# Kernel tuning notes

Measured on AMD Instinct MI355X. Metric: run time of the kernel, lower is better.

Reference implementation:

```python
import jax, jax.numpy as jnp
import numpy as np

BERT_DIM, HIDDEN, LABELS, UFD = 768, 256, 9, 20
B, R, S = 64, 16, 64


def _masked_mean(x, mask, axis):
    # x: [..., axis, d], mask: [..., axis] float 0/1 -> masked mean over `axis`
    num = jnp.sum(x * mask[..., None], axis=axis)
    den = jnp.maximum(jnp.sum(mask, axis=axis), 1e-9)[..., None]
    return num / den


def setup_inputs() -> dict:
    key = jax.random.key(0)
    ks = jax.random.split(key, 8)
    sc = 0.02
    return {
        "inputs": jax.random.normal(ks[0], (B, R, S, BERT_DIM), jnp.float32),
        "user_feats": jax.random.normal(ks[1], (B, UFD), jnp.float32),
        "W_proj": jax.random.normal(ks[2], (BERT_DIM, HIDDEN), jnp.float32) * sc,
        "b_proj": jnp.zeros((HIDDEN,), jnp.float32),
        "W_rff": jax.random.normal(ks[3], (HIDDEN + UFD, 1), jnp.float32) * sc,
        "b_rff": jnp.zeros((1,), jnp.float32),
        "W_pff": jax.random.normal(ks[4], (HIDDEN + UFD, LABELS), jnp.float32) * sc,
        "b_pff": jnp.zeros((LABELS,), jnp.float32),
        "user_w": jnp.ones((UFD,), jnp.float32),
    }


def reference(inputs, user_feats, W_proj, b_proj, W_rff, b_rff, W_pff, b_pff, user_w):
    # projection: [B,R,S,bert] -> [B,R,S,H]
    x = jnp.einsum("brsd,dh->brsh", inputs, W_proj) + b_proj
    # sentence-level DAN: mask = sum over hidden != 0 (as in source, post-projection)
    s_mask = (jnp.sum(x, axis=-1) != 0).astype(x.dtype)          # [B,R,S]
    r_hn = _masked_mean(x, s_mask, axis=2)                        # [B,R,H]
    # review-level DAN
    r_mask = (jnp.sum(x, axis=(-1, -2)) != 0).astype(x.dtype)    # [B,R]
    p_hn = _masked_mean(r_hn, r_mask, axis=1)                     # [B,H]
    # F.normalize(user_feats) (L2 over dim=1, eps=1e-12) scaled by learned weights
    nrm = jnp.maximum(jnp.linalg.norm(user_feats, axis=1, keepdims=True), 1e-12)
    uf = (user_feats / nrm) * user_w
    p_batch = jnp.concatenate([p_hn, uf], axis=-1)                # [B,H+UFD]
    # review feedforward (Linear -> SELU), squeezed -> [B]
    r_stars = jax.nn.selu(p_batch @ W_rff + b_rff)[:, 0]
    # product DAN over the batch axis (no mask -> plain mean), then Linear+SELU
    h_n = jnp.mean(p_batch, axis=0)                               # [H+UFD]
    p_stars = jax.nn.selu(h_n @ W_pff + b_pff)                    # [LABELS]
    return p_stars, r_stars
```

## Files before the change

kernel.cpp:

```cpp
#include <hip/hip_runtime.h>
#include <cmath>

static constexpr int BERT   = 768;
static constexpr int HID    = 256;
static constexpr int NLAB   = 9;
static constexpr int NUFD   = 20;
static constexpr int NB     = 64;
static constexpr int NR     = 16;
static constexpr int NS     = 64;
static constexpr int PBD    = HID + NUFD;

static constexpr size_t WS_A      = 0;
static constexpr size_t WS_COLSUM = 786432;
static constexpr size_t WS_SUMB   = 787200;
static constexpr size_t WS_CNT    = 787264;
static constexpr size_t WS_TSUM   = 788288;
static constexpr size_t WS_PB     = 789312;

__device__ __forceinline__ float selu_f(float x) {
    const float alpha = 1.6732632423543772848170429916717f;
    const float scale = 1.0507009873554804934193349852946f;
    return scale * (x > 0.0f ? x : alpha * (expf(x) - 1.0f));
}

__global__ __launch_bounds__(256) void k0_colsum(
    const float* __restrict__ W, const float* __restrict__ bp,
    float* __restrict__ colsum, float* __restrict__ sumb) {
    int blk = blockIdx.x;
    int tid = threadIdx.x;
    if (blk < 3) {
        int d = blk * 256 + tid;
        const float4* W4 = (const float4*)W;
        float4 s4 = make_float4(0.f, 0.f, 0.f, 0.f);
        for (int h4 = 0; h4 < HID / 4; ++h4) {
            float4 v = W4[(size_t)d * (HID / 4) + h4];
            s4.x += v.x; s4.y += v.y; s4.z += v.z; s4.w += v.w;
        }
        colsum[d] = (s4.x + s4.y) + (s4.z + s4.w);
    } else {
        __shared__ float red[256];
        red[tid] = bp[tid];
        __syncthreads();
        for (int s = 128; s > 0; s >>= 1) {
            if (tid < s) red[tid] += red[tid + s];
            __syncthreads();
        }
        if (tid == 0) *sumb = red[0];
    }
}

__global__ __launch_bounds__(256) void k1_reduce(
    const float* __restrict__ inp, const float* __restrict__ colsum,
    const float* __restrict__ sumb, float* __restrict__ A,
    float* __restrict__ cnt_g, float* __restrict__ tsum_g) {
    int br  = blockIdx.x;
    int tid = threadIdx.x;
    int w = tid >> 6, l = tid & 63;

    const float4* cs4 = (const float4*)colsum;
    float4 c0 = cs4[l], c1 = cs4[64 + l], c2 = cs4[128 + l];
    float sb = *sumb;

    const float4* base = (const float4*)(inp + (size_t)br * NS * BERT);
    float4 a0 = make_float4(0.f,0.f,0.f,0.f);
    float4 a1 = make_float4(0.f,0.f,0.f,0.f);
    float4 a2 = make_float4(0.f,0.f,0.f,0.f);
    float cnt = 0.f, ts = 0.f;

    #pragma unroll 4
    for (int i = 0; i < 16; ++i) {
        int s = w * 16 + i;
        const float4* rp = base + (size_t)s * (BERT / 4);
        float4 v0 = rp[l];
        float4 v1 = rp[64 + l];
        float4 v2 = rp[128 + l];
        float p = v0.x*c0.x + v0.y*c0.y + v0.z*c0.z + v0.w*c0.w
                + v1.x*c1.x + v1.y*c1.y + v1.z*c1.z + v1.w*c1.w
                + v2.x*c2.x + v2.y*c2.y + v2.z*c2.z + v2.w*c2.w;
        #pragma unroll
        for (int off = 32; off > 0; off >>= 1) p += __shfl_xor(p, off);
        float t = p + sb;
        ts += t;
        if (t != 0.0f) {
            a0.x += v0.x; a0.y += v0.y; a0.z += v0.z; a0.w += v0.w;
            a1.x += v1.x; a1.y += v1.y; a1.z += v1.z; a1.w += v1.w;
            a2.x += v2.x; a2.y += v2.y; a2.z += v2.z; a2.w += v2.w;
            cnt += 1.0f;
        }
    }

    __shared__ float part[4][BERT];
    __shared__ float cw[4], tw[4];
    float* pw = part[w];
    ((float4*)pw)[l]       = a0;
    ((float4*)pw)[64 + l]  = a1;
    ((float4*)pw)[128 + l] = a2;
    if (l == 0) { cw[w] = cnt; tw[w] = ts; }
    __syncthreads();

    float* Ao = A + (size_t)br * BERT;
    for (int c = tid; c < BERT; c += 256)
        Ao[c] = (part[0][c] + part[1][c]) + (part[2][c] + part[3][c]);
    if (tid == 0) {
        cnt_g[br]  = (cw[0] + cw[1]) + (cw[2] + cw[3]);
        tsum_g[br] = (tw[0] + tw[1]) + (tw[2] + tw[3]);
    }
}

__global__ __launch_bounds__(256) void k2_perb(
    const float* __restrict__ A, const float* __restrict__ cnt_g,
    const float* __restrict__ tsum_g, const float* __restrict__ W_proj,
    const float* __restrict__ b_proj, const float* __restrict__ user_feats,
    const float* __restrict__ user_w, const float* __restrict__ W_rff,
    const float* __restrict__ b_rff, float* __restrict__ pb_out,
    float* __restrict__ r_out) {
    int b   = blockIdx.x;
    int tid = threadIdx.x;

    __shared__ float M[BERT];
    __shared__ float g[NR];
    __shared__ float scal[4];
    __shared__ float pb[PBD];
    __shared__ float red[256];

    if (tid < NR) {
        float c  = cnt_g[b * NR + tid];
        float t  = tsum_g[b * NR + tid];
        float rm = (t != 0.0f) ? 1.0f : 0.0f;
        float den = fmaxf(c, 1e-9f);
        g[tid]       = rm / den;
        red[tid]     = rm;
        red[16 + tid] = rm * (c / den);
    }
    __syncthreads();
    if (tid == 0) {
        float srm = 0.f, sq = 0.f;
        for (int r = 0; r < NR; ++r) { srm += red[r]; sq += red[16 + r]; }
        scal[0] = fmaxf(srm, 1e-9f);
        scal[1] = sq;
    }
    for (int c = tid; c < BERT; c += 256) {
        float m = 0.f;
        #pragma unroll
        for (int r = 0; r < NR; ++r)
            m += g[r] * A[(size_t)(b * NR + r) * BERT + c];
        M[c] = m;
    }
    __syncthreads();

    float acc = 0.f;
    {
        const float* Wc = W_proj + tid;
        #pragma unroll 8
        for (int d = 0; d < BERT; ++d) acc += M[d] * Wc[(size_t)d * HID];
    }
    pb[tid] = (acc + b_proj[tid] * scal[1]) / scal[0];

    if (tid < NUFD) red[tid] = user_feats[b * NUFD + tid];
    __syncthreads();
    if (tid == 0) {
        float s = 0.f;
        for (int j = 0; j < NUFD; ++j) s += red[j] * red[j];
        scal[2] = 1.0f / fmaxf(sqrtf(s), 1e-12f);
    }
    __syncthreads();
    if (tid < NUFD) pb[HID + tid] = red[tid] * scal[2] * user_w[tid];
    __syncthreads();

    pb_out[b * PBD + tid] = pb[tid];
    if (tid < PBD - HID) pb_out[b * PBD + HID + tid] = pb[HID + tid];

    float part = pb[tid] * W_rff[tid];
    if (tid < PBD - HID) part += pb[HID + tid] * W_rff[HID + tid];
    red[tid] = part;
    __syncthreads();
    for (int s = 128; s > 0; s >>= 1) {
        if (tid < s) red[tid] += red[tid + s];
        __syncthreads();
    }
    if (tid == 0) r_out[b] = selu_f(red[0] + b_rff[0]);
}

__global__ __launch_bounds__(320) void k3_final(
    const float* __restrict__ pb, const float* __restrict__ W_pff,
    const float* __restrict__ b_pff, float* __restrict__ out) {
    __shared__ float hn[PBD];
    int tid = threadIdx.x;
    if (tid < PBD) {
        float s = 0.f;
        for (int b = 0; b < NB; ++b) s += pb[b * PBD + tid];
        hn[tid] = s * (1.0f / NB);
    }
    __syncthreads();
    if (tid < NLAB) {
        float acc = 0.f;
        for (int j = 0; j < PBD; ++j) acc += hn[j] * W_pff[j * NLAB + tid];
        out[tid] = selu_f(acc + b_pff[tid]);
    }
}

extern "C" void kernel_launch(void* const* d_in, const int* in_sizes, int n_in,
                              void* d_out, int out_size, void* d_ws, size_t ws_size,
                              hipStream_t stream) {
    const float* inputs     = (const float*)d_in[0];
    const float* user_feats = (const float*)d_in[1];
    const float* W_proj     = (const float*)d_in[2];
    const float* b_proj     = (const float*)d_in[3];
    const float* W_rff      = (const float*)d_in[4];
    const float* b_rff      = (const float*)d_in[5];
    const float* W_pff      = (const float*)d_in[6];
    const float* b_pff      = (const float*)d_in[7];
    const float* user_w     = (const float*)d_in[8];
    float* out = (float*)d_out;
    float* ws  = (float*)d_ws;

    float* A      = ws + WS_A;
    float* colsum = ws + WS_COLSUM;
    float* sumb   = ws + WS_SUMB;
    float* cntg   = ws + WS_CNT;
    float* tsumg  = ws + WS_TSUM;
    float* pb     = ws + WS_PB;

    hipLaunchKernelGGL(k0_colsum, dim3(4), dim3(256), 0, stream,
                       W_proj, b_proj, colsum, sumb);
    hipLaunchKernelGGL(k1_reduce, dim3(NB * NR), dim3(256), 0, stream,
                       inputs, colsum, sumb, A, cntg, tsumg);
    hipLaunchKernelGGL(k2_perb, dim3(NB), dim3(256), 0, stream,
                       A, cntg, tsumg, W_proj, b_proj, user_feats, user_w,
                       W_rff, b_rff, pb, out + NLAB);
    hipLaunchKernelGGL(k3_final, dim3(1), dim3(320), 0, stream,
                       pb, W_pff, b_pff, out);
}
```

Measured before the change: 345.1 us.

## Split per-batch projection GEMV across four blocks and use nontemporal input loads

The per-batch projection kernel now runs four blocks per batch row. Each block computes 64 hidden outputs, with a 4-way split-K over the 768 input dims reduced in shared memory, replacing one block doing a full 768-long loop per thread. The review feedforward (r_stars) moves into the final single-block kernel, computed by 64 threads. The main streaming reduction reads inputs with nontemporal loads and uses native vector types. This raises parallelism in the small GEMV stage but recomputes the M vector four times per batch row.

```diff
diff --git a/kernel.cpp b/kernel.cpp
--- a/kernel.cpp
+++ b/kernel.cpp
@@ -10,6 +10,8 @@
 static constexpr int NS     = 64;
 static constexpr int PBD    = HID + NUFD;
 
+typedef float v4f __attribute__((ext_vector_type(4)));
+
 static constexpr size_t WS_A      = 0;
 static constexpr size_t WS_COLSUM = 786432;
 static constexpr size_t WS_SUMB   = 787200;
@@ -30,12 +32,11 @@
     int tid = threadIdx.x;
     if (blk < 3) {
         int d = blk * 256 + tid;
-        const float4* W4 = (const float4*)W;
-        float4 s4 = make_float4(0.f, 0.f, 0.f, 0.f);
-        for (int h4 = 0; h4 < HID / 4; ++h4) {
-            float4 v = W4[(size_t)d * (HID / 4) + h4];
-            s4.x += v.x; s4.y += v.y; s4.z += v.z; s4.w += v.w;
-        }
+        const v4f* W4 = (const v4f*)W;
+        v4f s4 = {0.f, 0.f, 0.f, 0.f};
+        #pragma unroll 8
+        for (int h4 = 0; h4 < HID / 4; ++h4)
+            s4 += W4[(size_t)d * (HID / 4) + h4];
         colsum[d] = (s4.x + s4.y) + (s4.z + s4.w);
     } else {
         __shared__ float red[256];
@@ -57,23 +58,23 @@
     int tid = threadIdx.x;
     int w = tid >> 6, l = tid & 63;
 
-    const float4* cs4 = (const float4*)colsum;
-    float4 c0 = cs4[l], c1 = cs4[64 + l], c2 = cs4[128 + l];
+    const v4f* cs4 = (const v4f*)colsum;
+    v4f c0 = cs4[l], c1 = cs4[64 + l], c2 = cs4[128 + l];
     float sb = *sumb;
 
-    const float4* base = (const float4*)(inp + (size_t)br * NS * BERT);
-    float4 a0 = make_float4(0.f,0.f,0.f,0.f);
-    float4 a1 = make_float4(0.f,0.f,0.f,0.f);
-    float4 a2 = make_float4(0.f,0.f,0.f,0.f);
+    const v4f* base = (const v4f*)(inp + (size_t)br * NS * BERT);
+    v4f a0 = {0.f,0.f,0.f,0.f};
+    v4f a1 = {0.f,0.f,0.f,0.f};
+    v4f a2 = {0.f,0.f,0.f,0.f};
     float cnt = 0.f, ts = 0.f;
 
     #pragma unroll 4
     for (int i = 0; i < 16; ++i) {
         int s = w * 16 + i;
-        const float4* rp = base + (size_t)s * (BERT / 4);
-        float4 v0 = rp[l];
-        float4 v1 = rp[64 + l];
-        float4 v2 = rp[128 + l];
+        const v4f* rp = base + (size_t)s * (BERT / 4);
+        v4f v0 = __builtin_nontemporal_load(rp + l);
+        v4f v1 = __builtin_nontemporal_load(rp + 64 + l);
+        v4f v2 = __builtin_nontemporal_load(rp + 128 + l);
         float p = v0.x*c0.x + v0.y*c0.y + v0.z*c0.z + v0.w*c0.w
                 + v1.x*c1.x + v1.y*c1.y + v1.z*c1.z + v1.w*c1.w
                 + v2.x*c2.x + v2.y*c2.y + v2.z*c2.z + v2.w*c2.w;
@@ -82,9 +83,7 @@
         float t = p + sb;
         ts += t;
         if (t != 0.0f) {
-            a0.x += v0.x; a0.y += v0.y; a0.z += v0.z; a0.w += v0.w;
-            a1.x += v1.x; a1.y += v1.y; a1.z += v1.z; a1.w += v1.w;
-            a2.x += v2.x; a2.y += v2.y; a2.z += v2.z; a2.w += v2.w;
+            a0 += v0; a1 += v1; a2 += v2;
             cnt += 1.0f;
         }
     }
@@ -92,9 +91,9 @@
     __shared__ float part[4][BERT];
     __shared__ float cw[4], tw[4];
     float* pw = part[w];
-    ((float4*)pw)[l]       = a0;
-    ((float4*)pw)[64 + l]  = a1;
-    ((float4*)pw)[128 + l] = a2;
+    ((v4f*)pw)[l]       = a0;
+    ((v4f*)pw)[64 + l]  = a1;
+    ((v4f*)pw)[128 + l] = a2;
     if (l == 0) { cw[w] = cnt; tw[w] = ts; }
     __syncthreads();
 
@@ -107,20 +106,18 @@
     }
 }
 
-__global__ __launch_bounds__(256) void k2_perb(
+__global__ __launch_bounds__(256) void k2_gemm(
     const float* __restrict__ A, const float* __restrict__ cnt_g,
     const float* __restrict__ tsum_g, const float* __restrict__ W_proj,
     const float* __restrict__ b_proj, const float* __restrict__ user_feats,
-    const float* __restrict__ user_w, const float* __restrict__ W_rff,
-    const float* __restrict__ b_rff, float* __restrict__ pb_out,
-    float* __restrict__ r_out) {
-    int b   = blockIdx.x;
+    const float* __restrict__ user_w, float* __restrict__ pb_out) {
+    int b   = blockIdx.x >> 2;
+    int q   = blockIdx.x & 3;
     int tid = threadIdx.x;
 
     __shared__ float M[BERT];
     __shared__ float g[NR];
-    __shared__ float scal[4];
-    __shared__ float pb[PBD];
+    __shared__ float scal[2];
     __shared__ float red[256];
 
     if (tid < NR) {
@@ -128,14 +125,14 @@
         float t  = tsum_g[b * NR + tid];
         float rm = (t != 0.0f) ? 1.0f : 0.0f;
         float den = fmaxf(c, 1e-9f);
-        g[tid]       = rm / den;
-        red[tid]     = rm;
-        red[16 + tid] = rm * (c / den);
+        g[tid]        = rm / den;
+        red[tid]      = rm;
+        red[NR + tid] = rm * (c / den);
     }
     __syncthreads();
     if (tid == 0) {
         float srm = 0.f, sq = 0.f;
-        for (int r = 0; r < NR; ++r) { srm += red[r]; sq += red[16 + r]; }
+        for (int r = 0; r < NR; ++r) { srm += red[r]; sq += red[NR + r]; }
         scal[0] = fmaxf(srm, 1e-9f);
         scal[1] = sq;
     }
@@ -148,54 +145,67 @@
     }
     __syncthreads();
 
-    float acc = 0.f;
+    int hl = tid & 63;
+    int ks = tid >> 6;
+    int h  = q * 64 + hl;
     {
-        const float* Wc = W_proj + tid;
-        #pragma unroll 8
-        for (int d = 0; d < BERT; ++d) acc += M[d] * Wc[(size_t)d * HID];
-    }
-    pb[tid] = (acc + b_proj[tid] * scal[1]) / scal[0];
-
-    if (tid < NUFD) red[tid] = user_feats[b * NUFD + tid];
-    __syncthreads();
-    if (tid == 0) {
-        float s = 0.f;
-        for (int j = 0; j < NUFD; ++j) s += red[j] * red[j];
-        scal[2] = 1.0f / fmaxf(sqrtf(s), 1e-12f);
-    }
-    __syncthreads();
-    if (tid < NUFD) pb[HID + tid] = red[tid] * scal[2] * user_w[tid];
-    __syncthreads();
-
-    pb_out[b * PBD + tid] = pb[tid];
-    if (tid < PBD - HID) pb_out[b * PBD + HID + tid] = pb[HID + tid];
-
-    float part = pb[tid] * W_rff[tid];
-    if (tid < PBD - HID) part += pb[HID + tid] * W_rff[HID + tid];
-    red[tid] = part;
-    __syncthreads();
-    for (int s = 128; s > 0; s >>= 1) {
-        if (tid < s) red[tid] += red[tid + s];
+        const float* Wc = W_proj + h;
+        float acc = 0.f;
+        int d0 = ks * 192;
+        #pragma unroll 16
+        for (int j = 0; j < 192; ++j)
+            acc += M[d0 + j] * Wc[(size_t)(d0 + j) * HID];
+        red[tid] = acc;
+    }
+    __syncthreads();
+    if (tid < 64) {
+        float s = (red[tid] + red[64 + tid]) + (red[128 + tid] + red[192 + tid]);
+        int hh = q * 64 + tid;
+        pb_out[b * PBD + hh] = (s + b_proj[hh] * scal[1]) / scal[0];
+    }
+
+    if (q == 0) {
         __syncthreads();
-    }
-    if (tid == 0) r_out[b] = selu_f(red[0] + b_rff[0]);
+        if (tid == 0) {
+            float s = 0.f;
+            for (int j = 0; j < NUFD; ++j) {
+                float v = user_feats[b * NUFD + j];
+                s += v * v;
+            }
+            red[0] = 1.0f / fmaxf(sqrtf(s), 1e-12f);
+        }
+        __syncthreads();
+        if (tid < NUFD)
+            pb_out[b * PBD + HID + tid] =
+                user_feats[b * NUFD + tid] * red[0] * user_w[tid];
+    }
 }
 
 __global__ __launch_bounds__(320) void k3_final(
-    const float* __restrict__ pb, const float* __restrict__ W_pff,
+    const float* __restrict__ pb, const float* __restrict__ W_rff,
+    const float* __restrict__ b_rff, const float* __restrict__ W_pff,
     const float* __restrict__ b_pff, float* __restrict__ out) {
     __shared__ float hn[PBD];
     int tid = threadIdx.x;
     if (tid < PBD) {
         float s = 0.f;
+        #pragma unroll 8
         for (int b = 0; b < NB; ++b) s += pb[b * PBD + tid];
         hn[tid] = s * (1.0f / NB);
     }
     __syncthreads();
-    if (tid < NLAB) {
+    if (tid < NB) {
+        int b = tid;
         float acc = 0.f;
-        for (int j = 0; j < PBD; ++j) acc += hn[j] * W_pff[j * NLAB + tid];
-        out[tid] = selu_f(acc + b_pff[tid]);
+        #pragma unroll 12
+        for (int j = 0; j < PBD; ++j) acc += pb[b * PBD + j] * W_rff[j];
+        out[NLAB + b] = selu_f(acc + b_rff[0]);
+    } else if (tid >= 64 && tid < 64 + NLAB) {
+        int lab = tid - 64;
+        float acc = 0.f;
+        #pragma unroll 12
+        for (int j = 0; j < PBD; ++j) acc += hn[j] * W_pff[j * NLAB + lab];
+        out[lab] = selu_f(acc + b_pff[lab]);
     }
 }
 
@@ -225,9 +235,8 @@
                        W_proj, b_proj, colsum, sumb);
     hipLaunchKernelGGL(k1_reduce, dim3(NB * NR), dim3(256), 0, stream,
                        inputs, colsum, sumb, A, cntg, tsumg);
-    hipLaunchKernelGGL(k2_perb, dim3(NB), dim3(256), 0, stream,
-                       A, cntg, tsumg, W_proj, b_proj, user_feats, user_w,
-                       W_rff, b_rff, pb, out + NLAB);
+    hipLaunchKernelGGL(k2_gemm, dim3(NB * 4), dim3(256), 0, stream,
+                       A, cntg, tsumg, W_proj, b_proj, user_feats, user_w, pb);
     hipLaunchKernelGGL(k3_final, dim3(1), dim3(320), 0, stream,
-                       pb, W_pff, b_pff, out);
-}
+                       pb, W_rff, b_rff, W_pff, b_pff, out);
+}
```

Measured after the change: 303.5 us. 1.14x faster.
